# Performance work log

Measured on AMD Instinct MI355X. Metric: run time of the kernel, lower is better.

The kernel has to match this reference:

```python
import jax, jax.numpy as jnp
import numpy as np
from jax import lax

DIM = 1024
HEADS = 16
HEAD_DIM = DIM // HEADS
BLOCK = 128          # block_size_q == block_size_kv
DECAY = 0.9          # decay_factor
SPIKE_TH = 0.5       # spike_threshold
K_WINNERS = 4        # k-winner-take-all along head_dim
HIDDEN = 4 * DIM     # SwiGLU hidden_mult=4.0
EPS = 1e-5


def _rmsnorm(x, w):
    norm = lax.rsqrt(jnp.mean(x * x, axis=-1, keepdims=True) + EPS)
    return w * x * norm


def _spike_kwta(k):
    # spiking threshold: pass activation only above SPIKE_TH
    k = jnp.where(k > SPIKE_TH, k, 0.0)
    # k-winners-take-all along head_dim
    thr = lax.top_k(k, K_WINNERS)[0][..., -1:]  # [B,T,H,1]
    return jnp.where(k >= thr, k, 0.0)


def _mix(h, Wr, Wk, Wv, Wo):
    # chunkwise (blockwise) decayed linear attention, RWKV-style
    B, T, _ = h.shape
    N = T // BLOCK
    r = jax.nn.sigmoid((h @ Wr).reshape(B, T, HEADS, HEAD_DIM))  # receptance
    k = _spike_kwta((h @ Wk).reshape(B, T, HEADS, HEAD_DIM))
    v = (h @ Wv).reshape(B, T, HEADS, HEAD_DIM)

    def chunks(a):  # [B,T,H,D] -> [N,B,L,H,D]
        return a.reshape(B, N, BLOCK, HEADS, HEAD_DIM).transpose(1, 0, 2, 3, 4)

    rc_all, kc_all, vc_all = chunks(r), chunks(k), chunks(v)

    t_idx = jnp.arange(BLOCK, dtype=h.dtype)
    w_in = (DECAY ** (t_idx + 1.0))[None, :, None, None]        # weight on incoming state
    w_out = (DECAY ** (BLOCK - 1.0 - t_idx))[None, :, None, None]  # weight into next state
    lm = t_idx[:, None] - t_idx[None, :]
    mask = jnp.where(lm >= 0, DECAY ** lm, 0.0)                 # [L,L] causal decay
    w_L = DECAY ** BLOCK

    def step(S, inp):
        rc, kc, vc = inp  # each [B,L,H,D]
        inter = jnp.einsum('blhd,bhde->blhe', rc * w_in, S)
        A = jnp.einsum('blhd,bmhd->bhlm', rc, kc) * mask
        intra = jnp.einsum('bhlm,bmhe->blhe', A, vc)
        S_new = w_L * S + jnp.einsum('blhd,blhe->bhde', kc * w_out, vc)
        return S_new, inter + intra

    S0 = jnp.zeros((B, HEADS, HEAD_DIM, HEAD_DIM), h.dtype)
    _, y = lax.scan(step, S0, (rc_all, kc_all, vc_all))  # y: [N,B,L,H,D]
    y = y.transpose(1, 0, 2, 3, 4).reshape(B, T, DIM)
    return y @ Wo


def setup_inputs() -> dict:
    key = jax.random.key(0)
    ks = jax.random.split(key, 9)
    s = 0.02
    return {
        'x': jax.random.normal(ks[0], (2, 1024, DIM), jnp.float32),
        'norm1_w': jnp.ones((DIM,), jnp.float32),
        'Wr': jax.random.normal(ks[1], (DIM, DIM), jnp.float32) * s,
        'Wk': jax.random.normal(ks[2], (DIM, DIM), jnp.float32) * s + 0.5,
        'Wv': jax.random.normal(ks[3], (DIM, DIM), jnp.float32) * s,
        'Wo': jax.random.normal(ks[4], (DIM, DIM), jnp.float32) * s,
        'norm2_w': jnp.ones((DIM,), jnp.float32),
        'w1': jax.random.normal(ks[5], (DIM, HIDDEN), jnp.float32) * s,
        'w2': jax.random.normal(ks[6], (DIM, HIDDEN), jnp.float32) * s,
        'w3': jax.random.normal(ks[7], (HIDDEN, DIM), jnp.float32) * s,
    }


def reference(x, norm1_w, Wr, Wk, Wv, Wo, norm2_w, w1, w2, w3):
    x = x + _mix(_rmsnorm(x, norm1_w), Wr, Wk, Wv, Wo)
    h = _rmsnorm(x, norm2_w)
    x = x + (jax.nn.silu(h @ w1) * (h @ w2)) @ w3
    return x
```

## Files before the change

kernel.cpp:

```cpp
#include <hip/hip_runtime.h>
#include <hip/hip_bf16.h>
#include <math.h>


#define DIMD 1024
#define BT   2048
#define HEADS 16
#define HD   64
#define CHUNK 128
#define NCHUNK 8
#define HIDDEN 4096
#define WL_128 1.3900845e-06f
#define LOG2D  (-0.15200309344504997f)

typedef __attribute__((ext_vector_type(4))) float f32x4;
typedef __attribute__((ext_vector_type(8))) short bf16x8;

__device__ __forceinline__ unsigned short f2bf(float f) {
    __hip_bfloat16 h = __float2bfloat16(f);
    return __builtin_bit_cast(unsigned short, h);
}
__device__ __forceinline__ float bf2f(unsigned short u) {
    __hip_bfloat16 h = __builtin_bit_cast(__hip_bfloat16, u);
    return __bfloat162float(h);
}
__device__ __forceinline__ void gload_lds16(const void* g, void* l) {
    __builtin_amdgcn_global_load_lds(
        (const __attribute__((address_space(1))) void*)g,
        (__attribute__((address_space(3))) void*)l,
        16, 0, 0);
}

__global__ __launch_bounds__(256) void prep_kernel(const float* __restrict__ x,
                                                   const float* __restrict__ norm1w,
                                                   const float* __restrict__ Wr,
                                                   const float* __restrict__ Wv,
                                                   const float* __restrict__ Wo,
                                                   const float* __restrict__ Wk,
                                                   const float* __restrict__ w1,
                                                   const float* __restrict__ w2,
                                                   const float* __restrict__ w3,
                                                   unsigned short* __restrict__ BtA,
                                                   unsigned short* __restrict__ wo_t,
                                                   unsigned short* __restrict__ wkB,
                                                   unsigned short* __restrict__ w1t,
                                                   unsigned short* __restrict__ w2t,
                                                   unsigned short* __restrict__ w3t,
                                                   unsigned short* __restrict__ hI) {
    __shared__ float t[64][65];
    __shared__ float red[4];
    int bid = blockIdx.x;
    if (bid < 4096) {
        const float* src; unsigned short* dst; int K, N, tile, mode = 0;
        if (bid < 256)       { src = Wr; dst = BtA;                 K = 1024; N = 1024; tile = bid; }
        else if (bid < 512)  { src = Wv; dst = BtA + 1024 * 1024;   K = 1024; N = 1024; tile = bid - 256; }
        else if (bid < 768)  { src = Wo; dst = wo_t;                K = 1024; N = 1024; tile = bid - 512; }
        else if (bid < 1024) { src = Wk; dst = wkB;                 K = 1024; N = 1024; tile = bid - 768; mode = 1; }
        else if (bid < 2048) { src = w1; dst = w1t; K = 1024; N = 4096; tile = bid - 1024; }
        else if (bid < 3072) { src = w2; dst = w2t; K = 1024; N = 4096; tile = bid - 2048; }
        else                 { src = w3; dst = w3t; K = 4096; N = 1024; tile = bid - 3072; }
        int xt = N >> 6;
        int bn = (tile % xt) << 6, bk = (tile / xt) << 6;
        int tx = threadIdx.x & 15, ty = threadIdx.x >> 4;
        #pragma unroll
        for (int i = 0; i < 4; ++i) {
            float4 v = *reinterpret_cast<const float4*>(&src[(size_t)(bk + ty + i * 16) * N + bn + tx * 4]);
            t[ty + i * 16][tx * 4 + 0] = v.x;
            t[ty + i * 16][tx * 4 + 1] = v.y;
            t[ty + i * 16][tx * 4 + 2] = v.z;
            t[ty + i * 16][tx * 4 + 3] = v.w;
        }
        __syncthreads();
        #pragma unroll
        for (int i = 0; i < 4; ++i) {
            int nrow = ty + i * 16;
            if (mode == 0) {
                ushort4 o;
                o.x = f2bf(t[tx * 4 + 0][nrow]);
                o.y = f2bf(t[tx * 4 + 1][nrow]);
                o.z = f2bf(t[tx * 4 + 2][nrow]);
                o.w = f2bf(t[tx * 4 + 3][nrow]);
                *reinterpret_cast<ushort4*>(&dst[(size_t)(bn + nrow) * K + bk + tx * 4]) = o;
            } else {
                ushort4 o0, o1;
                unsigned short* p0 = (unsigned short*)&o0;
                unsigned short* p1 = (unsigned short*)&o1;
                #pragma unroll
                for (int j = 0; j < 4; ++j) {
                    float val = t[tx * 4 + j][nrow];
                    unsigned short b0 = f2bf(val);
                    p0[j] = b0;
                    p1[j] = f2bf(val - bf2f(b0));
                }
                size_t rb = (size_t)(bn + nrow) * 3072;
                *reinterpret_cast<ushort4*>(&wkB[rb + bk + tx * 4]) = o0;
                *reinterpret_cast<ushort4*>(&wkB[rb + 1024 + bk + tx * 4]) = o1;
                *reinterpret_cast<ushort4*>(&wkB[rb + 2048 + bk + tx * 4]) = o0;
            }
        }
    } else {
        int row = bid - 4096;
        const float* xr = x + (size_t)row * DIMD;
        int i0 = threadIdx.x * 4;
        float4 v = *reinterpret_cast<const float4*>(xr + i0);
        float ss = v.x*v.x + v.y*v.y + v.z*v.z + v.w*v.w;
        #pragma unroll
        for (int off = 32; off; off >>= 1) ss += __shfl_xor(ss, off);
        if ((threadIdx.x & 63) == 0) red[threadIdx.x >> 6] = ss;
        __syncthreads();
        ss = red[0] + red[1] + red[2] + red[3];
        float norm = rsqrtf(ss * (1.0f / DIMD) + 1e-5f);
        float4 wv = *reinterpret_cast<const float4*>(norm1w + i0);
        float o[4];
        o[0] = wv.x * v.x * norm; o[1] = wv.y * v.y * norm;
        o[2] = wv.z * v.z * norm; o[3] = wv.w * v.w * norm;
        ushort4 u0, u1;
        unsigned short* q0 = (unsigned short*)&u0;
        unsigned short* q1 = (unsigned short*)&u1;
        #pragma unroll
        for (int j = 0; j < 4; ++j) {
            q0[j] = f2bf(o[j]);
            q1[j] = f2bf(o[j] - bf2f(q0[j]));
        }
        *reinterpret_cast<ushort4*>(hI + (size_t)row * 2048 + i0) = u0;
        *reinterpret_cast<ushort4*>(hI + (size_t)row * 2048 + 1024 + i0) = u1;
    }
}

__global__ __launch_bounds__(256) void proj_kernel(const unsigned short* __restrict__ hI,
                                                   const unsigned short* __restrict__ BtA,
                                                   const unsigned short* __restrict__ wkB,
                                                   unsigned short* __restrict__ r16,
                                                   unsigned short* __restrict__ v16,
                                                   unsigned short* __restrict__ k16) {
    __shared__ __align__(16) short As[128 * 64];
    __shared__ __align__(16) short Bs[128 * 64];
    const int tid = threadIdx.x;
    const int wv = tid >> 6, ln = tid & 63;
    const int g = ln >> 4, r = ln & 15;
    const int srow_off = ln >> 3;
    const int sslot = ln & 7;
    const short* Ag = (const short*)hI;

    if (blockIdx.x < 256) {
        const int bx = blockIdx.x & 15, by = blockIdx.x >> 4;
        const int bm = by << 7, bn = bx << 7;
        const int wr = (wv >> 1) << 6, wc = (wv & 1) << 6;
        const short* Bg = (const short*)BtA;
        f32x4 acc[4][4];
        #pragma unroll
        for (int i = 0; i < 4; ++i)
            #pragma unroll
            for (int j = 0; j < 4; ++j) acc[i][j] = (f32x4){0.f, 0.f, 0.f, 0.f};
        for (int k0 = 0; k0 < 1024; k0 += 64) {
            #pragma unroll
            for (int i = 0; i < 4; ++i) {
                int c = wv * 4 + i;
                int row = c * 8 + srow_off;
                int kcol = ((sslot ^ (row & 7)) << 3);
                gload_lds16(Ag + (size_t)(bm + row) * 2048 + k0 + kcol, &As[c * 512 + ln * 8]);
                gload_lds16(Bg + (size_t)(bn + row) * 1024 + k0 + kcol, &Bs[c * 512 + ln * 8]);
            }
            __syncthreads();
            #pragma unroll
            for (int kk = 0; kk < 2; ++kk) {
                bf16x8 af[4], bfr[4];
                #pragma unroll
                for (int mi = 0; mi < 4; ++mi) {
                    int row = wr + mi * 16 + r;
                    int slot = (kk * 4 + g) ^ (row & 7);
                    af[mi] = *reinterpret_cast<const bf16x8*>(&As[row * 64 + slot * 8]);
                }
                #pragma unroll
                for (int ni = 0; ni < 4; ++ni) {
                    int row = wc + ni * 16 + r;
                    int slot = (kk * 4 + g) ^ (row & 7);
                    bfr[ni] = *reinterpret_cast<const bf16x8*>(&Bs[row * 64 + slot * 8]);
                }
                #pragma unroll
                for (int mi = 0; mi < 4; ++mi)
                    #pragma unroll
                    for (int ni = 0; ni < 4; ++ni)
                        acc[mi][ni] = __builtin_amdgcn_mfma_f32_16x16x32_bf16(
                            af[mi], bfr[ni], acc[mi][ni], 0, 0, 0);
            }
            __syncthreads();
        }
        #pragma unroll
        for (int mi = 0; mi < 4; ++mi)
            #pragma unroll
            for (int q = 0; q < 4; ++q) {
                int row = bm + wr + mi * 16 + g * 4 + q;
                #pragma unroll
                for (int ni = 0; ni < 4; ++ni) {
                    int col = bn + wc + ni * 16 + r;
                    float vv = acc[mi][ni][q];
                    if (col < 1024) {
                        r16[(size_t)row * 1024 + col] = f2bf(1.0f / (1.0f + expf(-vv)));
                    } else {
                        v16[(size_t)row * 1024 + col - 1024] = f2bf(vv);
                    }
                }
            }
    } else {
        const int id = blockIdx.x - 256;
        const int bx = id & 7, by = id >> 3;
        const int bm = by << 6, bn = bx << 7;
        const int wr = (wv >> 1) << 5, wc = (wv & 1) << 6;
        const short* Bg = (const short*)wkB;
        f32x4 acc[2][4];
        #pragma unroll
        for (int i = 0; i < 2; ++i)
            #pragma unroll
            for (int j = 0; j < 4; ++j) acc[i][j] = (f32x4){0.f, 0.f, 0.f, 0.f};
        for (int k0 = 0; k0 < 3072; k0 += 64) {
            int srck0 = (k0 >= 1024) ? (k0 - 1024) : k0;
            #pragma unroll
            for (int i = 0; i < 2; ++i) {
                int c = wv * 2 + i;
                int row = c * 8 + srow_off;
                int kcol = ((sslot ^ (row & 7)) << 3);
                gload_lds16(Ag + (size_t)(bm + row) * 2048 + srck0 + kcol, &As[c * 512 + ln * 8]);
            }
            #pragma unroll
            for (int i = 0; i < 4; ++i) {
                int c = wv * 4 + i;
                int row = c * 8 + srow_off;
                int kcol = ((sslot ^ (row & 7)) << 3);
                gload_lds16(Bg + (size_t)(bn + row) * 3072 + k0 + kcol, &Bs[c * 512 + ln * 8]);
            }
            __syncthreads();
            #pragma unroll
            for (int kk = 0; kk < 2; ++kk) {
                bf16x8 af[2], bfr[4];
                #pragma unroll
                for (int mi = 0; mi < 2; ++mi) {
                    int row = wr + mi * 16 + r;
                    int slot = (kk * 4 + g) ^ (row & 7);
                    af[mi] = *reinterpret_cast<const bf16x8*>(&As[row * 64 + slot * 8]);
                }
                #pragma unroll
                for (int ni = 0; ni < 4; ++ni) {
                    int row = wc + ni * 16 + r;
                    int slot = (kk * 4 + g) ^ (row & 7);
                    bfr[ni] = *reinterpret_cast<const bf16x8*>(&Bs[row * 64 + slot * 8]);
                }
                #pragma unroll
                for (int mi = 0; mi < 2; ++mi)
                    #pragma unroll
                    for (int ni = 0; ni < 4; ++ni)
                        acc[mi][ni] = __builtin_amdgcn_mfma_f32_16x16x32_bf16(
                            af[mi], bfr[ni], acc[mi][ni], 0, 0, 0);
            }
            __syncthreads();
        }
        const unsigned long long gmask = 0xFFFFULL << (g * 16);
        #pragma unroll
        for (int mi = 0; mi < 2; ++mi) {
            #pragma unroll
            for (int q = 0; q < 4; ++q) {
                float s[4], cur[4];
                #pragma unroll
                for (int ni = 0; ni < 4; ++ni) {
                    float a = acc[mi][ni][q];
                    s[ni] = (a > 0.5f) ? a : 0.0f;
                    cur[ni] = s[ni];
                }
                float thr = 0.0f;
                #pragma unroll
                for (int it = 0; it < 4; ++it) {
                    float lm = fmaxf(fmaxf(cur[0], cur[1]), fmaxf(cur[2], cur[3]));
                    float gm = lm;
                    #pragma unroll
                    for (int off = 1; off < 16; off <<= 1) gm = fmaxf(gm, __shfl_xor(gm, off));
                    thr = gm;
                    unsigned long long ball = __ballot(lm == gm) & gmask;
                    int leader = __ffsll(ball) - 1;
                    if (ln == leader) {
                        bool done = false;
                        #pragma unroll
                        for (int ni = 0; ni < 4; ++ni) {
                            if (!done && cur[ni] == gm) { cur[ni] = -1.0f; done = true; }
                        }
                    }
                }
                int row = bm + wr + mi * 16 + g * 4 + q;
                #pragma unroll
                for (int ni = 0; ni < 4; ++ni) {
                    float o = (s[ni] >= thr) ? s[ni] : 0.0f;
                    k16[(size_t)row * 1024 + bn + wc + ni * 16 + r] = f2bf(o);
                }
            }
        }
    }
}

__global__ __launch_bounds__(256) void transpose_attn4(const unsigned short* __restrict__ v16,
                                                       const unsigned short* __restrict__ k16,
                                                       unsigned short* __restrict__ vTg,
                                                       unsigned short* __restrict__ kwTg) {
    __shared__ float t[64][65];
    int z = blockIdx.z;
    const unsigned short* src = (z < 2) ? v16 : k16;
    unsigned short* dst = (z < 2) ? vTg : kwTg;
    int b = z & 1;
    int scaled = (z >= 2);
    int bc = blockIdx.x * 64, bt = blockIdx.y * 64;
    int tx = threadIdx.x & 15, ty = threadIdx.x >> 4;
    #pragma unroll
    for (int i = 0; i < 4; ++i) {
        ushort4 v = *reinterpret_cast<const ushort4*>(&src[(size_t)(b * 1024 + bt + ty + i * 16) * 1024 + bc + tx * 4]);
        t[ty + i * 16][tx * 4 + 0] = bf2f(v.x);
        t[ty + i * 16][tx * 4 + 1] = bf2f(v.y);
        t[ty + i * 16][tx * 4 + 2] = bf2f(v.z);
        t[ty + i * 16][tx * 4 + 3] = bf2f(v.w);
    }
    __syncthreads();
    #pragma unroll
    for (int i = 0; i < 4; ++i) {
        int crow = ty + i * 16;
        ushort4 o;
        unsigned short* po = (unsigned short*)&o;
        #pragma unroll
        for (int j = 0; j < 4; ++j) {
            int tl = bt + tx * 4 + j;
            float sc = scaled ? exp2f((float)(127 - (tl & 127)) * LOG2D) : 1.0f;
            po[j] = f2bf(t[tx * 4 + j][crow] * sc);
        }
        *reinterpret_cast<ushort4*>(&dst[(size_t)(b * 1024 + bc + crow) * 1024 + bt + tx * 4]) = o;
    }
}

template <int EPI, int MI>
__global__ __launch_bounds__(256) void gemm_bf16(const unsigned short* __restrict__ A,
                                                 const unsigned short* __restrict__ Bt,
                                                 void* __restrict__ Cout,
                                                 const float* __restrict__ add,
                                                 int M, int N, int K) {
    __shared__ __align__(16) short As[MI * 32 * 64];
    __shared__ __align__(16) short Bs[128 * 64];
    const int tid = threadIdx.x;
    const int wv = tid >> 6, ln = tid & 63;
    const int bm = blockIdx.y * (MI * 32), bn = blockIdx.x << 7;
    const int wr = (wv >> 1) * (MI * 16), wc = (wv & 1) << 6;
    const int g = ln >> 4, r16 = ln & 15;

    f32x4 acc[MI][4];
    #pragma unroll
    for (int i = 0; i < MI; ++i)
        #pragma unroll
        for (int j = 0; j < 4; ++j) acc[i][j] = (f32x4){0.f, 0.f, 0.f, 0.f};

    const short* Ag = (const short*)A;
    const short* Bg = (const short*)Bt;
    const int srow_off = ln >> 3;
    const int sslot = ln & 7;
    for (int k0 = 0; k0 < K; k0 += 64) {
        #pragma unroll
        for (int i = 0; i < MI; ++i) {
            int c = wv * MI + i;
            int row = c * 8 + srow_off;
            int kcol = ((sslot ^ (row & 7)) << 3);
            gload_lds16(Ag + (size_t)(bm + row) * K + k0 + kcol, &As[c * 512 + ln * 8]);
        }
        #pragma unroll
        for (int i = 0; i < 4; ++i) {
            int c = wv * 4 + i;
            int row = c * 8 + srow_off;
            int kcol = ((sslot ^ (row & 7)) << 3);
            gload_lds16(Bg + (size_t)(bn + row) * K + k0 + kcol, &Bs[c * 512 + ln * 8]);
        }
        __syncthreads();
        #pragma unroll
        for (int kk = 0; kk < 2; ++kk) {
            bf16x8 af[MI], bfr[4];
            #pragma unroll
            for (int mi = 0; mi < MI; ++mi) {
                int row = wr + mi * 16 + r16;
                int slot = (kk * 4 + g) ^ (row & 7);
                af[mi] = *reinterpret_cast<const bf16x8*>(&As[row * 64 + slot * 8]);
            }
            #pragma unroll
            for (int ni = 0; ni < 4; ++ni) {
                int row = wc + ni * 16 + r16;
                int slot = (kk * 4 + g) ^ (row & 7);
                bfr[ni] = *reinterpret_cast<const bf16x8*>(&Bs[row * 64 + slot * 8]);
            }
            #pragma unroll
            for (int mi = 0; mi < MI; ++mi)
                #pragma unroll
                for (int ni = 0; ni < 4; ++ni)
                    acc[mi][ni] = __builtin_amdgcn_mfma_f32_16x16x32_bf16(
                        af[mi], bfr[ni], acc[mi][ni], 0, 0, 0);
        }
        __syncthreads();
    }
    #pragma unroll
    for (int mi = 0; mi < MI; ++mi)
        #pragma unroll
        for (int q = 0; q < 4; ++q) {
            int row = bm + wr + mi * 16 + g * 4 + q;
            #pragma unroll
            for (int ni = 0; ni < 4; ++ni) {
                int col = bn + wc + ni * 16 + r16;
                float vv = acc[mi][ni][q];
                size_t o = (size_t)row * N + col;
                if (EPI == 2) vv += add[o];
                if (EPI == 3) ((unsigned short*)Cout)[o] = f2bf(vv);
                else          ((float*)Cout)[o] = vv;
            }
        }
}

__global__ __launch_bounds__(256) void gemm_splitk(const unsigned short* __restrict__ A,
                                                   const unsigned short* __restrict__ Bt,
                                                   float* __restrict__ P01,
                                                   float* __restrict__ P23,
                                                   int M, int N, int lda) {
    __shared__ __align__(16) short As[128 * 64];
    __shared__ __align__(16) short Bs[128 * 64];
    const int tid = threadIdx.x;
    const int wv = tid >> 6, ln = tid & 63;
    const int bm = blockIdx.y << 7, bn = blockIdx.x << 7;
    const int z = blockIdx.z;
    const int wr = (wv >> 1) << 6, wc = (wv & 1) << 6;
    const int g = ln >> 4, r16 = ln & 15;
    float* C = (z < 2) ? (P01 + (size_t)z * M * N) : (P23 + (size_t)(z - 2) * M * N);

    f32x4 acc[4][4];
    #pragma unroll
    for (int i = 0; i < 4; ++i)
        #pragma unroll
        for (int j = 0; j < 4; ++j) acc[i][j] = (f32x4){0.f, 0.f, 0.f, 0.f};

    const short* Ag = (const short*)A + z * 1024;
    const short* Bg = (const short*)Bt + z * 1024;
    const int srow_off = ln >> 3;
    const int sslot = ln & 7;
    for (int k0 = 0; k0 < 1024; k0 += 64) {
        #pragma unroll
        for (int i = 0; i < 4; ++i) {
            int c = wv * 4 + i;
            int row = c * 8 + srow_off;
            int kcol = ((sslot ^ (row & 7)) << 3);
            gload_lds16(Ag + (size_t)(bm + row) * lda + k0 + kcol, &As[c * 512 + ln * 8]);
            gload_lds16(Bg + (size_t)(bn + row) * lda + k0 + kcol, &Bs[c * 512 + ln * 8]);
        }
        __syncthreads();
        #pragma unroll
        for (int kk = 0; kk < 2; ++kk) {
            bf16x8 af[4], bfr[4];
            #pragma unroll
            for (int mi = 0; mi < 4; ++mi) {
                int row = wr + mi * 16 + r16;
                int slot = (kk * 4 + g) ^ (row & 7);
                af[mi] = *reinterpret_cast<const bf16x8*>(&As[row * 64 + slot * 8]);
            }
            #pragma unroll
            for (int ni = 0; ni < 4; ++ni) {
                int row = wc + ni * 16 + r16;
                int slot = (kk * 4 + g) ^ (row & 7);
                bfr[ni] = *reinterpret_cast<const bf16x8*>(&Bs[row * 64 + slot * 8]);
            }
            #pragma unroll
            for (int mi = 0; mi < 4; ++mi)
                #pragma unroll
                for (int ni = 0; ni < 4; ++ni)
                    acc[mi][ni] = __builtin_amdgcn_mfma_f32_16x16x32_bf16(
                        af[mi], bfr[ni], acc[mi][ni], 0, 0, 0);
        }
        __syncthreads();
    }
    #pragma unroll
    for (int mi = 0; mi < 4; ++mi)
        #pragma unroll
        for (int q = 0; q < 4; ++q) {
            int row = bm + wr + mi * 16 + g * 4 + q;
            #pragma unroll
            for (int ni = 0; ni < 4; ++ni)
                C[(size_t)row * N + bn + wc + ni * 16 + r16] = acc[mi][ni][q];
        }
}

__global__ __launch_bounds__(256) void reduce4_kernel(float* __restrict__ out,
                                                      const float* __restrict__ p0,
                                                      const float* __restrict__ p1,
                                                      const float* __restrict__ p2,
                                                      const float* __restrict__ p3) {
    size_t i = ((size_t)blockIdx.x * 256 + threadIdx.x) * 4;
    float4 o = *reinterpret_cast<float4*>(&out[i]);
    float4 a = *reinterpret_cast<const float4*>(&p0[i]);
    float4 b = *reinterpret_cast<const float4*>(&p1[i]);
    float4 c = *reinterpret_cast<const float4*>(&p2[i]);
    float4 d = *reinterpret_cast<const float4*>(&p3[i]);
    o.x += a.x + b.x + c.x + d.x;
    o.y += a.y + b.y + c.y + d.y;
    o.z += a.z + b.z + c.z + d.z;
    o.w += a.w + b.w + c.w + d.w;
    *reinterpret_cast<float4*>(&out[i]) = o;
}

__global__ __launch_bounds__(256) void gemm_swiglu_bf16(const unsigned short* __restrict__ A,
                                                        const unsigned short* __restrict__ B1t,
                                                        const unsigned short* __restrict__ B2t,
                                                        unsigned short* __restrict__ G,
                                                        int M, int N, int K) {
    __shared__ __align__(16) short As[128 * 64];
    __shared__ __align__(16) short Bs1[128 * 64];
    __shared__ __align__(16) short Bs2[128 * 64];
    const int tid = threadIdx.x;
    const int wv = tid >> 6, ln = tid & 63;
    const int bm = blockIdx.y << 7, bn = blockIdx.x << 7;
    const int wr = (wv >> 1) << 6, wc = (wv & 1) << 6;
    const int g = ln >> 4, r16 = ln & 15;

    f32x4 acc1[4][4], acc2[4][4];
    #pragma unroll
    for (int i = 0; i < 4; ++i)
        #pragma unroll
        for (int j = 0; j < 4; ++j) {
            acc1[i][j] = (f32x4){0.f, 0.f, 0.f, 0.f};
            acc2[i][j] = (f32x4){0.f, 0.f, 0.f, 0.f};
        }

    const short* Ag = (const short*)A;
    const short* B1g = (const short*)B1t;
    const short* B2g = (const short*)B2t;
    const int srow_off = ln >> 3;
    const int sslot = ln & 7;
    for (int k0 = 0; k0 < K; k0 += 64) {
        #pragma unroll
        for (int i = 0; i < 4; ++i) {
            int c = wv * 4 + i;
            int row = c * 8 + srow_off;
            int kcol = ((sslot ^ (row & 7)) << 3);
            gload_lds16(Ag + (size_t)(bm + row) * K + k0 + kcol, &As[c * 512 + ln * 8]);
            gload_lds16(B1g + (size_t)(bn + row) * K + k0 + kcol, &Bs1[c * 512 + ln * 8]);
            gload_lds16(B2g + (size_t)(bn + row) * K + k0 + kcol, &Bs2[c * 512 + ln * 8]);
        }
        __syncthreads();
        #pragma unroll
        for (int kk = 0; kk < 2; ++kk) {
            bf16x8 af[4], b1f[4], b2f[4];
            #pragma unroll
            for (int mi = 0; mi < 4; ++mi) {
                int row = wr + mi * 16 + r16;
                int slot = (kk * 4 + g) ^ (row & 7);
                af[mi] = *reinterpret_cast<const bf16x8*>(&As[row * 64 + slot * 8]);
            }
            #pragma unroll
            for (int ni = 0; ni < 4; ++ni) {
                int row = wc + ni * 16 + r16;
                int slot = (kk * 4 + g) ^ (row & 7);
                b1f[ni] = *reinterpret_cast<const bf16x8*>(&Bs1[row * 64 + slot * 8]);
                b2f[ni] = *reinterpret_cast<const bf16x8*>(&Bs2[row * 64 + slot * 8]);
            }
            #pragma unroll
            for (int mi = 0; mi < 4; ++mi)
                #pragma unroll
                for (int ni = 0; ni < 4; ++ni) {
                    acc1[mi][ni] = __builtin_amdgcn_mfma_f32_16x16x32_bf16(
                        af[mi], b1f[ni], acc1[mi][ni], 0, 0, 0);
                    acc2[mi][ni] = __builtin_amdgcn_mfma_f32_16x16x32_bf16(
                        af[mi], b2f[ni], acc2[mi][ni], 0, 0, 0);
                }
        }
        __syncthreads();
    }
    #pragma unroll
    for (int mi = 0; mi < 4; ++mi)
        #pragma unroll
        for (int q = 0; q < 4; ++q) {
            int row = bm + wr + mi * 16 + g * 4 + q;
            #pragma unroll
            for (int ni = 0; ni < 4; ++ni) {
                int col = bn + wc + ni * 16 + r16;
                float a = acc1[mi][ni][q];
                float vv = a / (1.0f + expf(-a)) * acc2[mi][ni][q];
                G[(size_t)row * N + col] = f2bf(vv);
            }
        }
}

__global__ __launch_bounds__(256) void rms2_kernel(const float* __restrict__ x,
                                                   const float* __restrict__ w,
                                                   unsigned short* __restrict__ h) {
    int row = blockIdx.x;
    const float* xr = x + (size_t)row * DIMD;
    int i0 = threadIdx.x * 4;
    float4 v = *reinterpret_cast<const float4*>(xr + i0);
    float ss = v.x*v.x + v.y*v.y + v.z*v.z + v.w*v.w;
    #pragma unroll
    for (int off = 32; off; off >>= 1) ss += __shfl_xor(ss, off);
    __shared__ float red[4];
    if ((threadIdx.x & 63) == 0) red[threadIdx.x >> 6] = ss;
    __syncthreads();
    ss = red[0] + red[1] + red[2] + red[3];
    float norm = rsqrtf(ss * (1.0f / DIMD) + 1e-5f);
    float4 wv = *reinterpret_cast<const float4*>(w + i0);
    ushort4 u;
    u.x = f2bf(wv.x * v.x * norm);
    u.y = f2bf(wv.y * v.y * norm);
    u.z = f2bf(wv.z * v.z * norm);
    u.w = f2bf(wv.w * v.w * norm);
    *reinterpret_cast<ushort4*>(h + (size_t)row * DIMD + i0) = u;
}

__global__ __launch_bounds__(256) void attn_state_mfma(const unsigned short* __restrict__ vTg,
                                                       const unsigned short* __restrict__ kwTg,
                                                       float* __restrict__ Cbuf) {
    __shared__ __align__(16) short vT_l[64 * 128];
    __shared__ __align__(16) short kwT_l[64 * 128];
    const int tid = threadIdx.x, w = tid >> 6, ln = tid & 63;
    const int n = blockIdx.x >> 5, bh = blockIdx.x & 31;
    const int b = bh >> 4, h = bh & 15;
    const int g = ln >> 4, r = ln & 15;
    const short* vg = (const short*)vTg;
    const short* kg = (const short*)kwTg;
    #pragma unroll
    for (int i = 0; i < 4; ++i) {
        int c = w * 4 + i;
        int row = c * 4 + (ln >> 4);
        int gs = (ln & 15) ^ (row & 7);
        size_t go = (size_t)(b * 1024 + h * 64 + row) * 1024 + n * 128 + gs * 8;
        gload_lds16(vg + go, &vT_l[c * 512 + ln * 8]);
        gload_lds16(kg + go, &kwT_l[c * 512 + ln * 8]);
    }
    __syncthreads();
    f32x4 acc[4];
    #pragma unroll
    for (int i = 0; i < 4; ++i) acc[i] = (f32x4){0.f, 0.f, 0.f, 0.f};
    #pragma unroll
    for (int ks = 0; ks < 4; ++ks) {
        int row_e = w * 16 + r;
        int se = (ks * 4 + g) ^ (row_e & 7);
        bf16x8 av = *reinterpret_cast<const bf16x8*>(&vT_l[row_e * 128 + se * 8]);
        #pragma unroll
        for (int ni = 0; ni < 4; ++ni) {
            int row_d = ni * 16 + r;
            int sd = (ks * 4 + g) ^ (row_d & 7);
            bf16x8 bk = *reinterpret_cast<const bf16x8*>(&kwT_l[row_d * 128 + sd * 8]);
            acc[ni] = __builtin_amdgcn_mfma_f32_16x16x32_bf16(av, bk, acc[ni], 0, 0, 0);
        }
    }
    size_t base = (size_t)blockIdx.x * 4096;
    #pragma unroll
    for (int ni = 0; ni < 4; ++ni)
        #pragma unroll
        for (int q = 0; q < 4; ++q) {
            int e = w * 16 + g * 4 + q;
            int d = ni * 16 + r;
            Cbuf[base + e * 64 + d] = acc[ni][q];
        }
}

__global__ __launch_bounds__(256) void attn_scan_kernel(const float* __restrict__ Cbuf,
                                                        unsigned short* __restrict__ STg) {
    int bh = blockIdx.x;
// ... 131 lines not shown
            for (int ei = 0; ei < 4; ++ei) yacc[mi][ei][q] *= win;
        }
    __syncthreads();
    #pragma unroll
    for (int ks = 0; ks < 4; ++ks) {
        bf16x8 ap[2];
        #pragma unroll
        for (int mi = 0; mi < 2; ++mi) {
            int row_l = w * 32 + mi * 16 + r;
            int s = (ks * 4 + g) ^ (row_l & 7);
            ap[mi] = *reinterpret_cast<const bf16x8*>(&PA_l[row_l * 128 + s * 8]);
        }
        #pragma unroll
        for (int ei = 0; ei < 4; ++ei) {
            int row_e = ei * 16 + r;
            int s = (ks * 4 + g) ^ (row_e & 7);
            bf16x8 bv = *reinterpret_cast<const bf16x8*>(&vT_l[row_e * 128 + s * 8]);
            #pragma unroll
            for (int mi = 0; mi < 2; ++mi)
                yacc[mi][ei] = __builtin_amdgcn_mfma_f32_16x16x32_bf16(ap[mi], bv, yacc[mi][ei], 0, 0, 0);
        }
    }
    #pragma unroll
    for (int mi = 0; mi < 2; ++mi)
        #pragma unroll
        for (int q = 0; q < 4; ++q) {
            int l = w * 32 + mi * 16 + g * 4 + q;
            size_t base = (size_t)(b * 1024 + n * 128 + l) * 1024 + h * 64;
            #pragma unroll
            for (int ei = 0; ei < 4; ++ei)
                y[base + ei * 16 + r] = f2bf(yacc[mi][ei][q]);
        }
}

extern "C" void kernel_launch(void* const* d_in, const int* in_sizes, int n_in,
                              void* d_out, int out_size, void* d_ws, size_t ws_size,
                              hipStream_t stream) {
    const float* x      = (const float*)d_in[0];
    const float* norm1w = (const float*)d_in[1];
    const float* Wr     = (const float*)d_in[2];
    const float* Wk     = (const float*)d_in[3];
    const float* Wv     = (const float*)d_in[4];
    const float* Wo     = (const float*)d_in[5];
    const float* norm2w = (const float*)d_in[6];
    const float* w1     = (const float*)d_in[7];
    const float* w2     = (const float*)d_in[8];
    const float* w3     = (const float*)d_in[9];
    float* out = (float*)d_out;
    char* ws = (char*)d_ws;
    (void)in_sizes; (void)n_in; (void)out_size; (void)ws_size;

    const size_t MB = 1048576;
    unsigned short* BtA  = (unsigned short*)(ws + 0 * MB);
    unsigned short* wkB  = (unsigned short*)(ws + 4 * MB);
    unsigned short* wo_t = (unsigned short*)(ws + 10 * MB);
    unsigned short* w1t  = (unsigned short*)(ws + 12 * MB);
    unsigned short* w2t  = (unsigned short*)(ws + 20 * MB);
    unsigned short* w3t  = (unsigned short*)(ws + 28 * MB);
    unsigned short* hI   = (unsigned short*)(ws + 36 * MB);
    unsigned short* r16  = (unsigned short*)(ws + 44 * MB);
    unsigned short* v16  = (unsigned short*)(ws + 48 * MB);
    unsigned short* k16  = (unsigned short*)(ws + 52 * MB);
    unsigned short* vTg  = (unsigned short*)(ws + 56 * MB);
    unsigned short* kwTg = (unsigned short*)(ws + 60 * MB);
    float*          Cbuf = (float*)(ws + 64 * MB);
    unsigned short* STg  = (unsigned short*)(ws + 68 * MB);
    unsigned short* y16  = (unsigned short*)(ws + 70 * MB);
    unsigned short* h0b  = (unsigned short*)(ws + 36 * MB);
    unsigned short* g16  = (unsigned short*)(ws + 56 * MB);
    float*          p01  = (float*)(ws + 12 * MB);
    float*          p23  = (float*)(ws + 40 * MB);

    dim3 blk(256);

    prep_kernel<<<6144, blk, 0, stream>>>(x, norm1w, Wr, Wv, Wo, Wk, w1, w2, w3,
                                          BtA, wo_t, wkB, w1t, w2t, w3t, hI);
    proj_kernel<<<512, blk, 0, stream>>>(hI, BtA, wkB, r16, v16, k16);
    transpose_attn4<<<dim3(16, 16, 4), blk, 0, stream>>>(v16, k16, vTg, kwTg);
    attn_state_mfma<<<NCHUNK * 32, blk, 0, stream>>>(vTg, kwTg, Cbuf);
    attn_scan_kernel<<<32, blk, 0, stream>>>(Cbuf, STg);
    attn_out_mfma<<<NCHUNK * 32, blk, 0, stream>>>(r16, k16, vTg, STg, y16);
    gemm_bf16<2, 2><<<dim3(8, 32), blk, 0, stream>>>(y16, wo_t, out, x, BT, DIMD, DIMD);
    rms2_kernel<<<BT, blk, 0, stream>>>(out, norm2w, h0b);
    gemm_swiglu_bf16<<<dim3(32, 16), blk, 0, stream>>>(h0b, w1t, w2t, g16, BT, HIDDEN, DIMD);
    gemm_splitk<<<dim3(8, 16, 4), blk, 0, stream>>>(g16, w3t, p01, p23, BT, DIMD, HIDDEN);
    reduce4_kernel<<<2048, blk, 0, stream>>>(out, p01, p01 + (size_t)BT * DIMD,
                                             p23, p23 + (size_t)BT * DIMD);
}
```

Baseline: 213.9 us.

## Double-buffer LDS staging with 32-wide K tiles across all GEMM kernels

```diff
diff --git a/kernel.cpp b/kernel.cpp
--- a/kernel.cpp
+++ b/kernel.cpp
@@ -29,6 +29,22 @@
         (const __attribute__((address_space(1))) void*)g,
         (__attribute__((address_space(3))) void*)l,
         16, 0, 0);
+}
+
+template <int NC>
+__device__ __forceinline__ void stage32(const short* __restrict__ src, int ld, int k0,
+                                        short* buf, int wv, int ln) {
+    int lrow = ln >> 2, lslot = ln & 3;
+    #pragma unroll
+    for (int i = 0; i < NC; ++i) {
+        int c = wv * NC + i;
+        int row = c * 16 + lrow;
+        int col8 = lslot ^ ((row >> 1) & 3);
+        gload_lds16(src + (size_t)row * ld + k0 + col8 * 8, buf + c * 512 + ln * 8);
+    }
+}
+__device__ __forceinline__ bf16x8 frag32(const short* buf, int row, int g) {
+    return *reinterpret_cast<const bf16x8*>(&buf[row * 32 + ((g ^ ((row >> 1) & 3)) << 3)]);
 }
 
 __global__ __launch_bounds__(256) void prep_kernel(const float* __restrict__ x,
@@ -133,57 +149,43 @@
                                                    unsigned short* __restrict__ r16,
                                                    unsigned short* __restrict__ v16,
                                                    unsigned short* __restrict__ k16) {
-    __shared__ __align__(16) short As[128 * 64];
-    __shared__ __align__(16) short Bs[128 * 64];
+    __shared__ __align__(16) short SA[2][4096];
+    __shared__ __align__(16) short SB[2][4096];
     const int tid = threadIdx.x;
     const int wv = tid >> 6, ln = tid & 63;
     const int g = ln >> 4, r = ln & 15;
-    const int srow_off = ln >> 3;
-    const int sslot = ln & 7;
-    const short* Ag = (const short*)hI;
 
     if (blockIdx.x < 256) {
         const int bx = blockIdx.x & 15, by = blockIdx.x >> 4;
         const int bm = by << 7, bn = bx << 7;
         const int wr = (wv >> 1) << 6, wc = (wv & 1) << 6;
-        const short* Bg = (const short*)BtA;
+        const short* Ag = (const short*)hI + (size_t)bm * 2048;
+        const short* Bg = (const short*)BtA + (size_t)bn * 1024;
         f32x4 acc[4][4];
         #pragma unroll
         for (int i = 0; i < 4; ++i)
             #pragma unroll
             for (int j = 0; j < 4; ++j) acc[i][j] = (f32x4){0.f, 0.f, 0.f, 0.f};
-        for (int k0 = 0; k0 < 1024; k0 += 64) {
-            #pragma unroll
-            for (int i = 0; i < 4; ++i) {
-                int c = wv * 4 + i;
-                int row = c * 8 + srow_off;
-                int kcol = ((sslot ^ (row & 7)) << 3);
-                gload_lds16(Ag + (size_t)(bm + row) * 2048 + k0 + kcol, &As[c * 512 + ln * 8]);
-                gload_lds16(Bg + (size_t)(bn + row) * 1024 + k0 + kcol, &Bs[c * 512 + ln * 8]);
+        stage32<2>(Ag, 2048, 0, SA[0], wv, ln);
+        stage32<2>(Bg, 1024, 0, SB[0], wv, ln);
+        __syncthreads();
+        for (int t = 0; t < 32; ++t) {
+            int cur = t & 1;
+            if (t + 1 < 32) {
+                stage32<2>(Ag, 2048, (t + 1) * 32, SA[cur ^ 1], wv, ln);
+                stage32<2>(Bg, 1024, (t + 1) * 32, SB[cur ^ 1], wv, ln);
             }
-            __syncthreads();
-            #pragma unroll
-            for (int kk = 0; kk < 2; ++kk) {
-                bf16x8 af[4], bfr[4];
+            bf16x8 af[4], bfr[4];
+            #pragma unroll
+            for (int mi = 0; mi < 4; ++mi) af[mi] = frag32(SA[cur], wr + mi * 16 + r, g);
+            #pragma unroll
+            for (int ni = 0; ni < 4; ++ni) bfr[ni] = frag32(SB[cur], wc + ni * 16 + r, g);
+            #pragma unroll
+            for (int mi = 0; mi < 4; ++mi)
                 #pragma unroll
-                for (int mi = 0; mi < 4; ++mi) {
-                    int row = wr + mi * 16 + r;
-                    int slot = (kk * 4 + g) ^ (row & 7);
-                    af[mi] = *reinterpret_cast<const bf16x8*>(&As[row * 64 + slot * 8]);
-                }
-                #pragma unroll
-                for (int ni = 0; ni < 4; ++ni) {
-                    int row = wc + ni * 16 + r;
-                    int slot = (kk * 4 + g) ^ (row & 7);
-                    bfr[ni] = *reinterpret_cast<const bf16x8*>(&Bs[row * 64 + slot * 8]);
-                }
-                #pragma unroll
-                for (int mi = 0; mi < 4; ++mi)
-                    #pragma unroll
-                    for (int ni = 0; ni < 4; ++ni)
-                        acc[mi][ni] = __builtin_amdgcn_mfma_f32_16x16x32_bf16(
-                            af[mi], bfr[ni], acc[mi][ni], 0, 0, 0);
-            }
+                for (int ni = 0; ni < 4; ++ni)
+                    acc[mi][ni] = __builtin_amdgcn_mfma_f32_16x16x32_bf16(
+                        af[mi], bfr[ni], acc[mi][ni], 0, 0, 0);
             __syncthreads();
         }
         #pragma unroll
@@ -207,69 +209,53 @@
         const int bx = id & 7, by = id >> 3;
         const int bm = by << 6, bn = bx << 7;
         const int wr = (wv >> 1) << 5, wc = (wv & 1) << 6;
-        const short* Bg = (const short*)wkB;
+        const short* Ag = (const short*)hI + (size_t)bm * 2048;
+        const short* Bg = (const short*)wkB + (size_t)bn * 3072;
         f32x4 acc[2][4];
         #pragma unroll
         for (int i = 0; i < 2; ++i)
             #pragma unroll
             for (int j = 0; j < 4; ++j) acc[i][j] = (f32x4){0.f, 0.f, 0.f, 0.f};
-        for (int k0 = 0; k0 < 3072; k0 += 64) {
-            int srck0 = (k0 >= 1024) ? (k0 - 1024) : k0;
-            #pragma unroll
-            for (int i = 0; i < 2; ++i) {
-                int c = wv * 2 + i;
-                int row = c * 8 + srow_off;
-                int kcol = ((sslot ^ (row & 7)) << 3);
-                gload_lds16(Ag + (size_t)(bm + row) * 2048 + srck0 + kcol, &As[c * 512 + ln * 8]);
+        stage32<1>(Ag, 2048, 0, SA[0], wv, ln);
+        stage32<2>(Bg, 3072, 0, SB[0], wv, ln);
+        __syncthreads();
+        for (int t = 0; t < 96; ++t) {
+            int cur = t & 1;
+            if (t + 1 < 96) {
+                int nk0 = (t + 1) * 32;
+                int srck0 = (nk0 >= 1024) ? (nk0 - 1024) : nk0;
+                stage32<1>(Ag, 2048, srck0, SA[cur ^ 1], wv, ln);
+                stage32<2>(Bg, 3072, nk0, SB[cur ^ 1], wv, ln);
             }
-            #pragma unroll
-            for (int i = 0; i < 4; ++i) {
-                int c = wv * 4 + i;
-                int row = c * 8 + srow_off;
-                int kcol = ((sslot ^ (row & 7)) << 3);
-                gload_lds16(Bg + (size_t)(bn + row) * 3072 + k0 + kcol, &Bs[c * 512 + ln * 8]);
-            }
+            bf16x8 af[2], bfr[4];
+            #pragma unroll
+            for (int mi = 0; mi < 2; ++mi) af[mi] = frag32(SA[cur], wr + mi * 16 + r, g);
+            #pragma unroll
+            for (int ni = 0; ni < 4; ++ni) bfr[ni] = frag32(SB[cur], wc + ni * 16 + r, g);
+            #pragma unroll
+            for (int mi = 0; mi < 2; ++mi)
+                #pragma unroll
+                for (int ni = 0; ni < 4; ++ni)
+                    acc[mi][ni] = __builtin_amdgcn_mfma_f32_16x16x32_bf16(
+                        af[mi], bfr[ni], acc[mi][ni], 0, 0, 0);
             __syncthreads();
-            #pragma unroll
-            for (int kk = 0; kk < 2; ++kk) {
-                bf16x8 af[2], bfr[4];
-                #pragma unroll
-                for (int mi = 0; mi < 2; ++mi) {
-                    int row = wr + mi * 16 + r;
-                    int slot = (kk * 4 + g) ^ (row & 7);
-                    af[mi] = *reinterpret_cast<const bf16x8*>(&As[row * 64 + slot * 8]);
-                }
-                #pragma unroll
-                for (int ni = 0; ni < 4; ++ni) {
-                    int row = wc + ni * 16 + r;
-                    int slot = (kk * 4 + g) ^ (row & 7);
-                    bfr[ni] = *reinterpret_cast<const bf16x8*>(&Bs[row * 64 + slot * 8]);
-                }
-                #pragma unroll
-                for (int mi = 0; mi < 2; ++mi)
-                    #pragma unroll
-                    for (int ni = 0; ni < 4; ++ni)
-                        acc[mi][ni] = __builtin_amdgcn_mfma_f32_16x16x32_bf16(
-                            af[mi], bfr[ni], acc[mi][ni], 0, 0, 0);
-            }
-            __syncthreads();
         }
         const unsigned long long gmask = 0xFFFFULL << (g * 16);
         #pragma unroll
         for (int mi = 0; mi < 2; ++mi) {
             #pragma unroll
             for (int q = 0; q < 4; ++q) {
-                float s[4], cur[4];
+                float s[4], cur4[4];
                 #pragma unroll
                 for (int ni = 0; ni < 4; ++ni) {
                     float a = acc[mi][ni][q];
                     s[ni] = (a > 0.5f) ? a : 0.0f;
-                    cur[ni] = s[ni];
+                    cur4[ni] = s[ni];
                 }
                 float thr = 0.0f;
                 #pragma unroll
                 for (int it = 0; it < 4; ++it) {
-                    float lm = fmaxf(fmaxf(cur[0], cur[1]), fmaxf(cur[2], cur[3]));
+                    float lm = fmaxf(fmaxf(cur4[0], cur4[1]), fmaxf(cur4[2], cur4[3]));
                     float gm = lm;
                     #pragma unroll
                     for (int off = 1; off < 16; off <<= 1) gm = fmaxf(gm, __shfl_xor(gm, off));
@@ -280,7 +266,7 @@
                         bool done = false;
                         #pragma unroll
                         for (int ni = 0; ni < 4; ++ni) {
-                            if (!done && cur[ni] == gm) { cur[ni] = -1.0f; done = true; }
+                            if (!done && cur4[ni] == gm) { cur4[ni] = -1.0f; done = true; }
                         }
                     }
                 }
@@ -337,8 +323,8 @@
                                                  void* __restrict__ Cout,
                                                  const float* __restrict__ add,
                                                  int M, int N, int K) {
-    __shared__ __align__(16) short As[MI * 32 * 64];
-    __shared__ __align__(16) short Bs[128 * 64];
+    __shared__ __align__(16) short SA[2][MI * 1024];
+    __shared__ __align__(16) short SB[2][4096];
     const int tid = threadIdx.x;
     const int wv = tid >> 6, ln = tid & 63;
     const int bm = blockIdx.y * (MI * 32), bn = blockIdx.x << 7;
@@ -351,48 +337,29 @@
         #pragma unroll
         for (int j = 0; j < 4; ++j) acc[i][j] = (f32x4){0.f, 0.f, 0.f, 0.f};
 
-    const short* Ag = (const short*)A;
-    const short* Bg = (const short*)Bt;
-    const int srow_off = ln >> 3;
-    const int sslot = ln & 7;
-    for (int k0 = 0; k0 < K; k0 += 64) {
-        #pragma unroll
-        for (int i = 0; i < MI; ++i) {
-            int c = wv * MI + i;
-            int row = c * 8 + srow_off;
-            int kcol = ((sslot ^ (row & 7)) << 3);
-            gload_lds16(Ag + (size_t)(bm + row) * K + k0 + kcol, &As[c * 512 + ln * 8]);
-        }
-        #pragma unroll
-        for (int i = 0; i < 4; ++i) {
-            int c = wv * 4 + i;
-            int row = c * 8 + srow_off;
-            int kcol = ((sslot ^ (row & 7)) << 3);
-            gload_lds16(Bg + (size_t)(bn + row) * K + k0 + kcol, &Bs[c * 512 + ln * 8]);
-        }
-        __syncthreads();
-        #pragma unroll
-        for (int kk = 0; kk < 2; ++kk) {
-            bf16x8 af[MI], bfr[4];
-            #pragma unroll
-            for (int mi = 0; mi < MI; ++mi) {
-                int row = wr + mi * 16 + r16;
-                int slot = (kk * 4 + g) ^ (row & 7);
-                af[mi] = *reinterpret_cast<const bf16x8*>(&As[row * 64 + slot * 8]);
-            }
-            #pragma unroll
-            for (int ni = 0; ni < 4; ++ni) {
-                int row = wc + ni * 16 + r16;
-                int slot = (kk * 4 + g) ^ (row & 7);
-                bfr[ni] = *reinterpret_cast<const bf16x8*>(&Bs[row * 64 + slot * 8]);
-            }
-            #pragma unroll
-            for (int mi = 0; mi < MI; ++mi)
-                #pragma unroll
-                for (int ni = 0; ni < 4; ++ni)
-                    acc[mi][ni] = __builtin_amdgcn_mfma_f32_16x16x32_bf16(
-                        af[mi], bfr[ni], acc[mi][ni], 0, 0, 0);
-        }
+    const short* Ag = (const short*)A + (size_t)bm * K;
+    const short* Bg = (const short*)Bt + (size_t)bn * K;
+    const int NT = K >> 5;
+    stage32<MI / 2>(Ag, K, 0, SA[0], wv, ln);
+    stage32<2>(Bg, K, 0, SB[0], wv, ln);
+    __syncthreads();
+    for (int t = 0; t < NT; ++t) {
+        int cur = t & 1;
+        if (t + 1 < NT) {
+            stage32<MI / 2>(Ag, K, (t + 1) * 32, SA[cur ^ 1], wv, ln);
+            stage32<2>(Bg, K, (t + 1) * 32, SB[cur ^ 1], wv, ln);
+        }
+        bf16x8 af[MI], bfr[4];
+        #pragma unroll
+        for (int mi = 0; mi < MI; ++mi) af[mi] = frag32(SA[cur], wr + mi * 16 + r16, g);
+        #pragma unroll
+        for (int ni = 0; ni < 4; ++ni) bfr[ni] = frag32(SB[cur], wc + ni * 16 + r16, g);
+        #pragma unroll
+        for (int mi = 0; mi < MI; ++mi)
+            #pragma unroll
+            for (int ni = 0; ni < 4; ++ni)
+                acc[mi][ni] = __builtin_amdgcn_mfma_f32_16x16x32_bf16(
+                    af[mi], bfr[ni], acc[mi][ni], 0, 0, 0);
         __syncthreads();
     }
     #pragma unroll
@@ -417,8 +384,8 @@
                                                    float* __restrict__ P01,
                                                    float* __restrict__ P23,
                                                    int M, int N, int lda) {
-    __shared__ __align__(16) short As[128 * 64];
-    __shared__ __align__(16) short Bs[128 * 64];
+    __shared__ __align__(16) short SA[2][4096];
+    __shared__ __align__(16) short SB[2][4096];
     const int tid = threadIdx.x;
     const int wv = tid >> 6, ln = tid & 63;
     const int bm = blockIdx.y << 7, bn = blockIdx.x << 7;
@@ -433,42 +400,28 @@
         #pragma unroll
         for (int j = 0; j < 4; ++j) acc[i][j] = (f32x4){0.f, 0.f, 0.f, 0.f};
 
-    const short* Ag = (const short*)A + z * 1024;
-    const short* Bg = (const short*)Bt + z * 1024;
-    const int srow_off = ln >> 3;
-    const int sslot = ln & 7;
-    for (int k0 = 0; k0 < 1024; k0 += 64) {
-        #pragma unroll
-        for (int i = 0; i < 4; ++i) {
-            int c = wv * 4 + i;
-            int row = c * 8 + srow_off;
-            int kcol = ((sslot ^ (row & 7)) << 3);
-            gload_lds16(Ag + (size_t)(bm + row) * lda + k0 + kcol, &As[c * 512 + ln * 8]);
-            gload_lds16(Bg + (size_t)(bn + row) * lda + k0 + kcol, &Bs[c * 512 + ln * 8]);
-        }
-        __syncthreads();
-        #pragma unroll
-        for (int kk = 0; kk < 2; ++kk) {
-            bf16x8 af[4], bfr[4];
-            #pragma unroll
-            for (int mi = 0; mi < 4; ++mi) {
-                int row = wr + mi * 16 + r16;
-                int slot = (kk * 4 + g) ^ (row & 7);
-                af[mi] = *reinterpret_cast<const bf16x8*>(&As[row * 64 + slot * 8]);
-            }
-            #pragma unroll
-            for (int ni = 0; ni < 4; ++ni) {
-                int row = wc + ni * 16 + r16;
-                int slot = (kk * 4 + g) ^ (row & 7);
-                bfr[ni] = *reinterpret_cast<const bf16x8*>(&Bs[row * 64 + slot * 8]);
-            }
-            #pragma unroll
-            for (int mi = 0; mi < 4; ++mi)
-                #pragma unroll
-                for (int ni = 0; ni < 4; ++ni)
-                    acc[mi][ni] = __builtin_amdgcn_mfma_f32_16x16x32_bf16(
-                        af[mi], bfr[ni], acc[mi][ni], 0, 0, 0);
-        }
+    const short* Ag = (const short*)A + (size_t)bm * lda + z * 1024;
+    const short* Bg = (const short*)Bt + (size_t)bn * lda + z * 1024;
+    stage32<2>(Ag, lda, 0, SA[0], wv, ln);
+    stage32<2>(Bg, lda, 0, SB[0], wv, ln);
+    __syncthreads();
+    for (int t = 0; t < 32; ++t) {
+        int cur = t & 1;
+        if (t + 1 < 32) {
+            stage32<2>(Ag, lda, (t + 1) * 32, SA[cur ^ 1], wv, ln);
+            stage32<2>(Bg, lda, (t + 1) * 32, SB[cur ^ 1], wv, ln);
+        }
+        bf16x8 af[4], bfr[4];
+        #pragma unroll
+        for (int mi = 0; mi < 4; ++mi) af[mi] = frag32(SA[cur], wr + mi * 16 + r16, g);
+        #pragma unroll
+        for (int ni = 0; ni < 4; ++ni) bfr[ni] = frag32(SB[cur], wc + ni * 16 + r16, g);
+        #pragma unroll
+        for (int mi = 0; mi < 4; ++mi)
+            #pragma unroll
+            for (int ni = 0; ni < 4; ++ni)
+                acc[mi][ni] = __builtin_amdgcn_mfma_f32_16x16x32_bf16(
+                    af[mi], bfr[ni], acc[mi][ni], 0, 0, 0);
         __syncthreads();
     }
     #pragma unroll
@@ -505,9 +458,9 @@
                                                         const unsigned short* __restrict__ B2t,
                                                         unsigned short* __restrict__ G,
                                                         int M, int N, int K) {
-    __shared__ __align__(16) short As[128 * 64];
-    __shared__ __align__(16) short Bs1[128 * 64];
-    __shared__ __align__(16) short Bs2[128 * 64];
+    __shared__ __align__(16) short SA[2][4096];
+    __shared__ __align__(16) short SB1[2][4096];
+    __shared__ __align__(16) short SB2[2][4096];
     const int tid = threadIdx.x;
     const int wv = tid >> 6, ln = tid & 63;
     const int bm = blockIdx.y << 7, bn = blockIdx.x << 7;
@@ -523,48 +476,38 @@
             acc2[i][j] = (f32x4){0.f, 0.f, 0.f, 0.f};
         }
 
-    const short* Ag = (const short*)A;
-    const short* B1g = (const short*)B1t;
-    const short* B2g = (const short*)B2t;
-    const int srow_off = ln >> 3;
-    const int sslot = ln & 7;
-    for (int k0 = 0; k0 < K; k0 += 64) {
-        #pragma unroll
-        for (int i = 0; i < 4; ++i) {
-            int c = wv * 4 + i;
-            int row = c * 8 + srow_off;
-            int kcol = ((sslot ^ (row & 7)) << 3);
-            gload_lds16(Ag + (size_t)(bm + row) * K + k0 + kcol, &As[c * 512 + ln * 8]);
-            gload_lds16(B1g + (size_t)(bn + row) * K + k0 + kcol, &Bs1[c * 512 + ln * 8]);
-            gload_lds16(B2g + (size_t)(bn + row) * K + k0 + kcol, &Bs2[c * 512 + ln * 8]);
-        }
-        __syncthreads();
-        #pragma unroll
-        for (int kk = 0; kk < 2; ++kk) {
-            bf16x8 af[4], b1f[4], b2f[4];
-            #pragma unroll
-            for (int mi = 0; mi < 4; ++mi) {
-                int row = wr + mi * 16 + r16;
-                int slot = (kk * 4 + g) ^ (row & 7);
-                af[mi] = *reinterpret_cast<const bf16x8*>(&As[row * 64 + slot * 8]);
+    const short* Ag  = (const short*)A + (size_t)bm * K;
+    const short* B1g = (const short*)B1t + (size_t)bn * K;
+    const short* B2g = (const short*)B2t + (size_t)bn * K;
+    const int NT = K >> 5;
+    stage32<2>(Ag, K, 0, SA[0], wv, ln);
+    stage32<2>(B1g, K, 0, SB1[0], wv, ln);
+    stage32<2>(B2g, K, 0, SB2[0], wv, ln);
+    __syncthreads();
+    for (int t = 0; t < NT; ++t) {
+        int cur = t & 1;
+        if (t + 1 < NT) {
+            stage32<2>(Ag, K, (t + 1) * 32, SA[cur ^ 1], wv, ln);
+            stage32<2>(B1g, K, (t + 1) * 32, SB1[cur ^ 1], wv, ln);
+            stage32<2>(B2g, K, (t + 1) * 32, SB2[cur ^ 1], wv, ln);
+        }
+        bf16x8 af[4], b1f[4], b2f[4];
+        #pragma unroll
+        for (int mi = 0; mi < 4; ++mi) af[mi] = frag32(SA[cur], wr + mi * 16 + r16, g);
+        #pragma unroll
+        for (int ni = 0; ni < 4; ++ni) {
+            b1f[ni] = frag32(SB1[cur], wc + ni * 16 + r16, g);
+            b2f[ni] = frag32(SB2[cur], wc + ni * 16 + r16, g);
+        }
+        #pragma unroll
+        for (int mi = 0; mi < 4; ++mi)
+            #pragma unroll
+            for (int ni = 0; ni < 4; ++ni) {
+                acc1[mi][ni] = __builtin_amdgcn_mfma_f32_16x16x32_bf16(
+                    af[mi], b1f[ni], acc1[mi][ni], 0, 0, 0);
+                acc2[mi][ni] = __builtin_amdgcn_mfma_f32_16x16x32_bf16(
+                    af[mi], b2f[ni], acc2[mi][ni], 0, 0, 0);
             }
-            #pragma unroll
-            for (int ni = 0; ni < 4; ++ni) {
-                int row = wc + ni * 16 + r16;
-                int slot = (kk * 4 + g) ^ (row & 7);
-                b1f[ni] = *reinterpret_cast<const bf16x8*>(&Bs1[row * 64 + slot * 8]);
-                b2f[ni] = *reinterpret_cast<const bf16x8*>(&Bs2[row * 64 + slot * 8]);
-            }
-            #pragma unroll
-            for (int mi = 0; mi < 4; ++mi)
-                #pragma unroll
-                for (int ni = 0; ni < 4; ++ni) {
-                    acc1[mi][ni] = __builtin_amdgcn_mfma_f32_16x16x32_bf16(
-                        af[mi], b1f[ni], acc1[mi][ni], 0, 0, 0);
-                    acc2[mi][ni] = __builtin_amdgcn_mfma_f32_16x16x32_bf16(
-                        af[mi], b2f[ni], acc2[mi][ni], 0, 0, 0);
-                }
-        }
         __syncthreads();
     }
     #pragma unroll
```

New measurement: 246.5 us. +15.2%, slower.

## Double-buffer SwiGLU GEMM LDS tiles and use 8 waves per block

Applied to the files above, without the earlier changes.

```diff
diff --git a/kernel.cpp b/kernel.cpp
--- a/kernel.cpp
+++ b/kernel.cpp
@@ -259,17 +259,17 @@
         for (int mi = 0; mi < 2; ++mi) {
             #pragma unroll
             for (int q = 0; q < 4; ++q) {
-                float s[4], cur[4];
+                float s[4], cur4[4];
                 #pragma unroll
                 for (int ni = 0; ni < 4; ++ni) {
                     float a = acc[mi][ni][q];
                     s[ni] = (a > 0.5f) ? a : 0.0f;
-                    cur[ni] = s[ni];
+                    cur4[ni] = s[ni];
                 }
                 float thr = 0.0f;
                 #pragma unroll
                 for (int it = 0; it < 4; ++it) {
-                    float lm = fmaxf(fmaxf(cur[0], cur[1]), fmaxf(cur[2], cur[3]));
+                    float lm = fmaxf(fmaxf(cur4[0], cur4[1]), fmaxf(cur4[2], cur4[3]));
                     float gm = lm;
                     #pragma unroll
                     for (int off = 1; off < 16; off <<= 1) gm = fmaxf(gm, __shfl_xor(gm, off));
@@ -280,7 +280,7 @@
                         bool done = false;
                         #pragma unroll
                         for (int ni = 0; ni < 4; ++ni) {
-                            if (!done && cur[ni] == gm) { cur[ni] = -1.0f; done = true; }
+                            if (!done && cur4[ni] == gm) { cur4[ni] = -1.0f; done = true; }
                         }
                     }
                 }
@@ -500,80 +500,96 @@
     *reinterpret_cast<float4*>(&out[i]) = o;
 }
 
-__global__ __launch_bounds__(256) void gemm_swiglu_bf16(const unsigned short* __restrict__ A,
+__global__ __launch_bounds__(512) void gemm_swiglu_bf16(const unsigned short* __restrict__ A,
                                                         const unsigned short* __restrict__ B1t,
                                                         const unsigned short* __restrict__ B2t,
                                                         unsigned short* __restrict__ G,
                                                         int M, int N, int K) {
-    __shared__ __align__(16) short As[128 * 64];
-    __shared__ __align__(16) short Bs1[128 * 64];
-    __shared__ __align__(16) short Bs2[128 * 64];
+    __shared__ __align__(16) short SA[2][8192];
+    __shared__ __align__(16) short SB1[2][8192];
+    __shared__ __align__(16) short SB2[2][8192];
     const int tid = threadIdx.x;
     const int wv = tid >> 6, ln = tid & 63;
     const int bm = blockIdx.y << 7, bn = blockIdx.x << 7;
-    const int wr = (wv >> 1) << 6, wc = (wv & 1) << 6;
+    const int wr = (wv >> 2) << 6, wc = (wv & 3) << 5;
     const int g = ln >> 4, r16 = ln & 15;
-
-    f32x4 acc1[4][4], acc2[4][4];
+    const int srow = ln >> 3, sslot = ln & 7;
+
+    f32x4 acc1[4][2], acc2[4][2];
     #pragma unroll
     for (int i = 0; i < 4; ++i)
         #pragma unroll
-        for (int j = 0; j < 4; ++j) {
+        for (int j = 0; j < 2; ++j) {
             acc1[i][j] = (f32x4){0.f, 0.f, 0.f, 0.f};
             acc2[i][j] = (f32x4){0.f, 0.f, 0.f, 0.f};
         }
 
-    const short* Ag = (const short*)A;
-    const short* B1g = (const short*)B1t;
-    const short* B2g = (const short*)B2t;
-    const int srow_off = ln >> 3;
-    const int sslot = ln & 7;
-    for (int k0 = 0; k0 < K; k0 += 64) {
-        #pragma unroll
-        for (int i = 0; i < 4; ++i) {
-            int c = wv * 4 + i;
-            int row = c * 8 + srow_off;
-            int kcol = ((sslot ^ (row & 7)) << 3);
-            gload_lds16(Ag + (size_t)(bm + row) * K + k0 + kcol, &As[c * 512 + ln * 8]);
-            gload_lds16(B1g + (size_t)(bn + row) * K + k0 + kcol, &Bs1[c * 512 + ln * 8]);
-            gload_lds16(B2g + (size_t)(bn + row) * K + k0 + kcol, &Bs2[c * 512 + ln * 8]);
-        }
-        __syncthreads();
+    const short* Ag  = (const short*)A + (size_t)bm * K;
+    const short* B1g = (const short*)B1t + (size_t)bn * K;
+    const short* B2g = (const short*)B2t + (size_t)bn * K;
+
+    #define SW_STAGE(k0, b)                                                        \
+        {                                                                          \
+            _Pragma("unroll")                                                      \
+            for (int i = 0; i < 2; ++i) {                                          \
+                int c = wv * 2 + i;                                                \
+                int row = c * 8 + srow;                                            \
+                int kc = ((sslot ^ (row & 7)) << 3);                               \
+                gload_lds16(Ag  + (size_t)row * K + (k0) + kc, &SA[b][c * 512 + ln * 8]);  \
+                gload_lds16(B1g + (size_t)row * K + (k0) + kc, &SB1[b][c * 512 + ln * 8]); \
+                gload_lds16(B2g + (size_t)row * K + (k0) + kc, &SB2[b][c * 512 + ln * 8]); \
+            }                                                                      \
+        }
+
+    const int NT = K >> 6;
+    SW_STAGE(0, 0);
+    asm volatile("s_waitcnt vmcnt(0)" ::: "memory");
+    __builtin_amdgcn_s_barrier();
+    asm volatile("" ::: "memory");
+    for (int t = 0; t < NT; ++t) {
+        int cur = t & 1;
+        if (t + 1 < NT) SW_STAGE((t + 1) << 6, cur ^ 1);
+        asm volatile("s_waitcnt vmcnt(6)" ::: "memory");
+        __builtin_amdgcn_s_barrier();
+        asm volatile("" ::: "memory");
         #pragma unroll
         for (int kk = 0; kk < 2; ++kk) {
-            bf16x8 af[4], b1f[4], b2f[4];
+            bf16x8 af[4], b1f[2], b2f[2];
             #pragma unroll
             for (int mi = 0; mi < 4; ++mi) {
                 int row = wr + mi * 16 + r16;
                 int slot = (kk * 4 + g) ^ (row & 7);
-                af[mi] = *reinterpret_cast<const bf16x8*>(&As[row * 64 + slot * 8]);
-            }
-            #pragma unroll
-            for (int ni = 0; ni < 4; ++ni) {
+                af[mi] = *reinterpret_cast<const bf16x8*>(&SA[cur][row * 64 + slot * 8]);
+            }
+            #pragma unroll
+            for (int ni = 0; ni < 2; ++ni) {
                 int row = wc + ni * 16 + r16;
                 int slot = (kk * 4 + g) ^ (row & 7);
-                b1f[ni] = *reinterpret_cast<const bf16x8*>(&Bs1[row * 64 + slot * 8]);
-                b2f[ni] = *reinterpret_cast<const bf16x8*>(&Bs2[row * 64 + slot * 8]);
+                b1f[ni] = *reinterpret_cast<const bf16x8*>(&SB1[cur][row * 64 + slot * 8]);
+                b2f[ni] = *reinterpret_cast<const bf16x8*>(&SB2[cur][row * 64 + slot * 8]);
             }
             #pragma unroll
             for (int mi = 0; mi < 4; ++mi)
                 #pragma unroll
-                for (int ni = 0; ni < 4; ++ni) {
+                for (int ni = 0; ni < 2; ++ni) {
                     acc1[mi][ni] = __builtin_amdgcn_mfma_f32_16x16x32_bf16(
                         af[mi], b1f[ni], acc1[mi][ni], 0, 0, 0);
                     acc2[mi][ni] = __builtin_amdgcn_mfma_f32_16x16x32_bf16(
                         af[mi], b2f[ni], acc2[mi][ni], 0, 0, 0);
                 }
         }
-        __syncthreads();
-    }
+        asm volatile("" ::: "memory");
+        __builtin_amdgcn_s_barrier();
+        asm volatile("" ::: "memory");
+    }
+    #undef SW_STAGE
     #pragma unroll
     for (int mi = 0; mi < 4; ++mi)
         #pragma unroll
         for (int q = 0; q < 4; ++q) {
             int row = bm + wr + mi * 16 + g * 4 + q;
             #pragma unroll
-            for (int ni = 0; ni < 4; ++ni) {
+            for (int ni = 0; ni < 2; ++ni) {
                 int col = bn + wc + ni * 16 + r16;
                 float a = acc1[mi][ni][q];
                 float vv = a / (1.0f + expf(-a)) * acc2[mi][ni][q];
@@ -871,7 +887,7 @@
     attn_out_mfma<<<NCHUNK * 32, blk, 0, stream>>>(r16, k16, vTg, STg, y16);
     gemm_bf16<2, 2><<<dim3(8, 32), blk, 0, stream>>>(y16, wo_t, out, x, BT, DIMD, DIMD);
     rms2_kernel<<<BT, blk, 0, stream>>>(out, norm2w, h0b);
-    gemm_swiglu_bf16<<<dim3(32, 16), blk, 0, stream>>>(h0b, w1t, w2t, g16, BT, HIDDEN, DIMD);
+    gemm_swiglu_bf16<<<dim3(32, 16), dim3(512), 0, stream>>>(h0b, w1t, w2t, g16, BT, HIDDEN, DIMD);
     gemm_splitk<<<dim3(8, 16, 4), blk, 0, stream>>>(g16, w3t, p01, p23, BT, DIMD, HIDDEN);
     reduce4_kernel<<<2048, blk, 0, stream>>>(out, p01, p01 + (size_t)BT * DIMD,
                                              p23, p23 + (size_t)BT * DIMD);
```

Result: faster. 201.1 us (-6.0%).
